# Kernel optimization log

Hardware: AMD Instinct MI355X
Metric: run time of the kernel (lower is better)

The kernel has to match this reference:

```python
import jax, jax.numpy as jnp
import numpy as np
import math

B, N, D, KA, H = 8, 1024, 512, 16, 8
QD = D // 4
HD = D // H


def qsplit(x):
    q = x.shape[-1] // 4
    return x[..., :q], x[..., q:2*q], x[..., 2*q:3*q], x[..., 3*q:]


def hprod(p, q):
    pr, pi, pj, pk = qsplit(p)
    qr, qi, qj, qk = qsplit(q)
    return jnp.concatenate([
        pr*qr - pi*qi - pj*qj - pk*qk,
        pr*qi + pi*qr + pj*qk - pk*qj,
        pr*qj - pi*qk + pj*qr + pk*qi,
        pr*qk + pi*qj - pj*qi + pk*qr,
    ], axis=-1)


def qconj(x):
    r, i, j, k = qsplit(x)
    return jnp.concatenate([r, -i, -j, -k], axis=-1)


def qlin(x, w, b):
    # w: [4, qo, qi] -> Hamilton block matrix [4qo, 4qi]
    r, i, j, k = w[0], w[1], w[2], w[3]
    W = jnp.concatenate([
        jnp.concatenate([r, -i, -j, -k], axis=1),
        jnp.concatenate([i,  r, -k,  j], axis=1),
        jnp.concatenate([j,  k,  r, -i], axis=1),
        jnp.concatenate([k, -j,  i,  r], axis=1),
    ], axis=0)
    return x @ W.T + b


def qln(x, gamma, beta):
    # per-component LayerNorm over Q; gamma/beta: [4, Q]
    qd = x.shape[-1] // 4
    xs = x.reshape(x.shape[:-1] + (4, qd))
    m = xs.mean(-1, keepdims=True)
    v = xs.var(-1, keepdims=True)
    y = (xs - m) / jnp.sqrt(v + 1e-5) * gamma + beta
    return y.reshape(x.shape)


def setup_inputs():
    key = jax.random.key(0)
    ks = jax.random.split(key, 20)
    lim = math.sqrt(6.0 / (2 * QD))  # xavier for [QD, QD]
    def qw(k):
        return jax.random.uniform(k, (4, QD, QD), minval=-lim, maxval=lim)
    return {
        'q': jax.random.normal(ks[0], (B, N, D), dtype=jnp.float32),
        'spike': jax.random.uniform(ks[1], (B, N), dtype=jnp.float32),
        'mask': jnp.ones((B, N), dtype=jnp.float32),
        'theta_logit': jnp.float32(0.0),
        'w_prim': qw(ks[2]), 'b_prim': jnp.zeros((D,), jnp.float32),
        'anchors': jax.random.normal(ks[3], (KA, D)) * 0.5,
        'log_sigma': jnp.zeros((KA,), jnp.float32),
        'w_aggr': qw(ks[4]), 'b_aggr': jnp.zeros((D,), jnp.float32),
        'w_q': qw(ks[5]), 'b_q': jnp.zeros((D,), jnp.float32),
        'w_k': qw(ks[6]), 'b_k': jnp.zeros((D,), jnp.float32),
        'w_v': qw(ks[7]), 'b_v': jnp.zeros((D,), jnp.float32),
        'w_o': qw(ks[8]), 'b_o': jnp.zeros((D,), jnp.float32),
        'ln_gamma': jnp.ones((4, QD), jnp.float32),
        'ln_beta': jnp.zeros((4, QD), jnp.float32),
    }


def reference(q, spike, mask, theta_logit, w_prim, b_prim, anchors, log_sigma,
              w_aggr, b_aggr, w_q, b_q, w_k, b_k, w_v, b_v, w_o, b_o,
              ln_gamma, ln_beta):
    b, n, d = q.shape
    qd = d // 4
    # --- SpikeQuaternionRotation: rotate toward K-axis by theta = theta_max*spike ---
    theta_max = (jnp.pi / 2) * jax.nn.sigmoid(theta_logit)
    theta = theta_max * spike                      # [B, N]
    c = jnp.cos(theta)[..., None]
    s = jnp.sin(theta)[..., None]
    z = jnp.zeros_like(c)
    rot = jnp.concatenate([
        jnp.broadcast_to(c, (b, n, qd)),
        jnp.broadcast_to(z, (b, n, qd)),
        jnp.broadcast_to(z, (b, n, qd)),
        jnp.broadcast_to(s, (b, n, qd)),
    ], axis=-1)
    q_rot = hprod(rot, q)                          # [B, N, D]

    # --- PrimaryLayer: per-cell quaternion transform ---
    msg_p = qlin(q_rot, w_prim, b_prim)

    # --- QuaternionAnchorLayer ---
    a_conj = qconj(anchors)                        # [KA, D]
    prod = hprod(q_rot[:, None, :, :], a_conj[None, :, None, :])  # [B, KA, N, D]
    dist = jnp.sum(prod * prod, axis=-1)           # [B, KA, N]
    sigma_sq = jnp.maximum(jnp.exp(log_sigma) ** 2, 1e-6)
    incid = jnp.exp(-dist / sigma_sq[None, :, None]) * mask[:, None, :]
    denom = jnp.maximum(incid.sum(-1, keepdims=True), 1e-6)
    h = jnp.einsum('bkn,bnd->bkd', incid, q_rot) / denom  # [B, KA, D]
    h = qlin(h, w_aggr, b_aggr)

    # --- QuaternionMHA(query=q_rot, key=h, value=h), no mask ---
    Qh = qlin(q_rot, w_q, b_q).reshape(b, n, H, HD)
    Kh = qlin(h, w_k, b_k).reshape(b, KA, H, HD)
    Vh = qlin(h, w_v, b_v).reshape(b, KA, H, HD)
    scores = jnp.einsum('bqhd,bkhd->bhqk', Qh, Kh) / jnp.sqrt(jnp.float32(HD))
    attn = jax.nn.softmax(scores, axis=-1)
    out = jnp.einsum('bhqk,bkhd->bqhd', attn, Vh).reshape(b, n, d)
    msg_a = qlin(out, w_o, b_o)

    # --- residual + per-component LayerNorm ---
    return qln(q + msg_p + msg_a, ln_gamma, ln_beta)
```

## Files before the change

### kernel.cpp

```cpp
#include <hip/hip_runtime.h>
#include <hip/hip_bf16.h>

typedef __hip_bfloat16 bf16;
typedef __attribute__((ext_vector_type(8))) short bf16x8;
typedef __attribute__((ext_vector_type(4))) float f32x4;

__device__ __forceinline__ float bflo(unsigned u) { return __uint_as_float(u << 16); }
__device__ __forceinline__ float bfhi(unsigned u) { return __uint_as_float(u & 0xffff0000u); }
__device__ __forceinline__ bool probe_f32(const void* mask) {
  return *(const unsigned*)mask == 0x3F800000u;
}
__device__ __forceinline__ float ldin(const void* p, size_t i, bool f32) {
  return f32 ? ((const float*)p)[i] : (float)((const bf16*)p)[i];
}

__global__ __launch_bounds__(256) void prologue(
    const void* w0, const void* w1, const void* w2, const void* w3,
    const void* w4, const void* w5,
    const void* b0, const void* b1, const void* b2, const void* b3,
    const void* b4, const void* b5, const void* g, const void* be,
    const void* q, const void* spike, const void* theta_logit, const void* mask,
    bf16* __restrict__ Wall, float* __restrict__ biasF,
    bf16* __restrict__ q_rot, float* __restrict__ qn) {
  bool f32 = probe_f32(mask);
  int blk = blockIdx.x, t = threadIdx.x;
  if (blk < 1536) {
    const int compT[4][4] = {{0,1,2,3},{1,0,3,2},{2,3,0,1},{3,2,1,0}};
    const float signT[4][4] = {{1.f,-1.f,-1.f,-1.f},{1.f,1.f,-1.f,1.f},{1.f,1.f,1.f,-1.f},{1.f,-1.f,1.f,1.f}};
    int E = blk * 1024 + t * 4;
    int wi = E >> 18;
    const void* src = wi == 0 ? w0 : wi == 1 ? w1 : wi == 2 ? w2 : wi == 3 ? w3 : wi == 4 ? w4 : w5;
    bf16 ov[4];
    #pragma unroll
    for (int j = 0; j < 4; ++j) {
      int e = (E + j) & 262143;
      int o = e >> 9, kk = e & 511;
      int ro = o >> 7, a = o & 127, co = kk >> 7, b2 = kk & 127;
      ov[j] = (bf16)(ldin(src, compT[ro][co] * 16384 + a * 128 + b2, f32) * signT[ro][co]);
    }
    *(uint2*)(Wall + E) = *(const uint2*)ov;
  } else if (blk < 1544) {
    int b = blk - 1536;
    const void* src = b == 0 ? b0 : b == 1 ? b1 : b == 2 ? b2 : b == 3 ? b3
                    : b == 4 ? b4 : b == 5 ? b5 : b == 6 ? g : be;
    biasF[b * 512 + t] = ldin(src, t, f32);
    biasF[b * 512 + 256 + t] = ldin(src, 256 + t, f32);
  } else {
    int row = (blk - 1544) * 2 + (t >> 7);
    int l = t & 127;
    float tl = ldin(theta_logit, 0, f32);
    float tmax = 1.5707963267948966f / (1.0f + __expf(-tl));
    float th = tmax * ldin(spike, row, f32);
    float c = cosf(th), s = sinf(th);
    size_t base = (size_t)row * 512;
    float a = ldin(q, base + l, f32), b = ldin(q, base + 128 + l, f32);
    float cc = ldin(q, base + 256 + l, f32), d = ldin(q, base + 384 + l, f32);
    float r0 = c * a - s * d;
    float r1 = c * b - s * cc;
    float r2 = c * cc + s * b;
    float r3 = c * d + s * a;
    bf16* orow = q_rot + base;
    orow[l] = (bf16)r0; orow[128 + l] = (bf16)r1; orow[256 + l] = (bf16)r2; orow[384 + l] = (bf16)r3;
    qn[(size_t)row * 128 + l] = r0 * r0 + r1 * r1 + r2 * r2 + r3 * r3;
  }
}

__device__ __forceinline__ void stage_B64(const bf16* __restrict__ Bw, int n0, char* Bs, int t) {
  int r = t & 63, cb = (t >> 6) * 16;
  const bf16* src = Bw + (size_t)(n0 + r) * 512;
  #pragma unroll
  for (int i = 0; i < 16; ++i) {
    int c = cb + i;
    int off = (c >> 2) * 4096 + (r >> 4) * 1024 + (((c & 3) * 16 + (r & 15)) * 16);
    *(uint4*)(Bs + off) = *(const uint4*)(src + c * 8);
  }
}

__global__ __launch_bounds__(256, 2) void gemm_dist(
    const bf16* __restrict__ A, const bf16* __restrict__ Bw,
    const float* __restrict__ bias0, const float* __restrict__ bias1,
    bf16* __restrict__ MQ,
    const float* __restrict__ qn, const void* anchors, const void* lsig,
    const void* mask, float* __restrict__ h_part, float* __restrict__ pd_part) {
  __shared__ char smem[77952];
  const int t = threadIdx.x;
  if (blockIdx.x >= 128) {
    char* Bs = smem;
    const int g = blockIdx.x - 128;
    const int wave = t >> 6, lane = t & 63;
    const int quad = lane >> 4, l16 = lane & 15;
    const int m0 = (g & 31) * 256, n0 = (g >> 5) * 64;
    stage_B64(Bw, n0, Bs, t);
    __syncthreads();
    const int mbase = m0 + wave * 64;
    f32x4 acc[4][4] = {};
    bf16x8 areg[2][4], breg[2][4];
    #pragma unroll
    for (int mt = 0; mt < 4; ++mt)
      areg[0][mt] = *(const bf16x8*)(A + (size_t)(mbase + mt * 16 + l16) * 512 + quad * 8);
    #pragma unroll
    for (int nt = 0; nt < 4; ++nt)
      breg[0][nt] = *(const bf16x8*)(Bs + nt * 1024 + lane * 16);
    #pragma unroll
    for (int kk = 0; kk < 16; ++kk) {
      const int cur = kk & 1, nxt = cur ^ 1;
      if (kk < 15) {
        const int k2 = (kk + 1) * 32;
        #pragma unroll
        for (int mt = 0; mt < 4; ++mt)
          areg[nxt][mt] = *(const bf16x8*)(A + (size_t)(mbase + mt * 16 + l16) * 512 + k2 + quad * 8);
        #pragma unroll
        for (int nt = 0; nt < 4; ++nt)
          breg[nxt][nt] = *(const bf16x8*)(Bs + (kk + 1) * 4096 + nt * 1024 + lane * 16);
      }
      #pragma unroll
      for (int mt = 0; mt < 4; ++mt)
        #pragma unroll
        for (int nt = 0; nt < 4; ++nt)
          acc[mt][nt] = __builtin_amdgcn_mfma_f32_16x16x32_bf16(areg[cur][mt], breg[cur][nt],
                                                                acc[mt][nt], 0, 0, 0);
    }
    #pragma unroll
    for (int nt = 0; nt < 4; ++nt) {
      int col = n0 + nt * 16 + l16;
      float bv = col < 512 ? bias0[col] : bias1[col - 512];
      #pragma unroll
      for (int mt = 0; mt < 4; ++mt) {
        int rb = mbase + mt * 16 + quad * 4;
        #pragma unroll
        for (int r = 0; r < 4; ++r)
          MQ[(size_t)(rb + r) * 1024 + col] = (bf16)(acc[mt][nt][r] + bv);
      }
    }
  } else {
    bool f32 = probe_f32(mask);
    bf16*  qr   = (bf16*)smem;
    float* an   = (float*)(smem + 65536);
    float* sInc = (float*)(smem + 73728);
    float* rs   = (float*)(smem + 77824);
    float* pd   = (float*)(smem + 77888);
    int bb = blockIdx.x;
    int b = bb >> 4, nc = bb & 15;
    {
      const uint4* src = (const uint4*)((const bf16*)A + ((size_t)b * 1024 + nc * 64) * 512);
      uint4* dst = (uint4*)qr;
      #pragma unroll
      for (int i = 0; i < 16; ++i) dst[t + i * 256] = src[t + i * 256];
    }
    for (int i = t; i < 2048; i += 256) {
      int k = i >> 7, l = i & 127;
      float a0 = ldin(anchors, k * 512 + l, f32);
      float a1 = ldin(anchors, k * 512 + 128 + l, f32);
      float a2 = ldin(anchors, k * 512 + 256 + l, f32);
      float a3 = ldin(anchors, k * 512 + 384 + l, f32);
      an[i] = a0 * a0 + a1 * a1 + a2 * a2 + a3 * a3;
    }
    if (t < 16) {
      float ls = ldin(lsig, t, f32);
      float ssq = __expf(ls); ssq = fmaxf(ssq * ssq, 1e-6f);
      rs[t] = -1.0f / ssq;
      pd[t] = 0.0f;
    }
    __syncthreads();
    {
      int rl = t >> 2, part = t & 3;
      int n = nc * 64 + rl;
      const float* qrow = qn + ((size_t)b * 1024 + n) * 128 + part * 32;
      f32x4 q4[8];
      #pragma unroll
      for (int i = 0; i < 8; ++i) q4[i] = *(const f32x4*)(qrow + i * 4);
      float sc[16] = {};
      #pragma unroll
      for (int i = 0; i < 8; ++i) {
        #pragma unroll
        for (int k = 0; k < 16; ++k) {
          f32x4 av = *(const f32x4*)(an + k * 128 + part * 32 + i * 4);
          sc[k] += q4[i][0] * av[0] + q4[i][1] * av[1] + q4[i][2] * av[2] + q4[i][3] * av[3];
        }
      }
      #pragma unroll
      for (int k = 0; k < 16; ++k) {
        sc[k] += __shfl_xor(sc[k], 1, 64);
        sc[k] += __shfl_xor(sc[k], 2, 64);
      }
      if (part == 0) {
        float mval = ldin(mask, b * 1024 + n, f32);
        #pragma unroll
        for (int k = 0; k < 16; ++k) {
          float inc = __expf(sc[k] * rs[k]) * mval;
          sInc[k * 64 + rl] = inc;
          atomicAdd(&pd[k], inc);
        }
      }
    }
    __syncthreads();
    {
      float acc0[16] = {}, acc1[16] = {};
      for (int nn = 0; nn < 64; ++nn) {
        float v0 = (float)qr[nn * 512 + t];
        float v1 = (float)qr[nn * 512 + 256 + t];
        #pragma unroll
        for (int k = 0; k < 16; ++k) {
          float p = sInc[k * 64 + nn];
          acc0[k] += p * v0;
          acc1[k] += p * v1;
        }
      }
      #pragma unroll
      for (int k = 0; k < 16; ++k) {
        size_t base = ((size_t)(b * 16 + k) * 16 + nc) * 512;
        h_part[base + t] = acc0[k];
        h_part[base + 256 + t] = acc1[k];
      }
    }
    if (t < 16) pd_part[((size_t)(b * 16 + t)) * 16 + nc] = pd[t];
  }
}

__global__ __launch_bounds__(256, 2) void gemm2(
    const bf16* __restrict__ A, const bf16* __restrict__ Bw,
    const float* __restrict__ biasO, bf16* __restrict__ msg_a) {
  __shared__ char Bs[65536];
  const int t = threadIdx.x;
  const int wave = t >> 6, lane = t & 63;
  const int quad = lane >> 4, l16 = lane & 15;
  const int m0 = blockIdx.x * 128, n0 = blockIdx.y * 64;
  stage_B64(Bw, n0, Bs, t);
  __syncthreads();
  const int mbase = m0 + wave * 32;
  f32x4 acc[2][4] = {};
  bf16x8 areg[2][2], breg[2][4];
  #pragma unroll
  for (int mt = 0; mt < 2; ++mt)
    areg[0][mt] = *(const bf16x8*)(A + (size_t)(mbase + mt * 16 + l16) * 512 + quad * 8);
  #pragma unroll
  for (int nt = 0; nt < 4; ++nt)
    breg[0][nt] = *(const bf16x8*)(Bs + nt * 1024 + lane * 16);
  #pragma unroll
  for (int kk = 0; kk < 16; ++kk) {
    const int cur = kk & 1, nxt = cur ^ 1;
    if (kk < 15) {
      const int k2 = (kk + 1) * 32;
      #pragma unroll
      for (int mt = 0; mt < 2; ++mt)
        areg[nxt][mt] = *(const bf16x8*)(A + (size_t)(mbase + mt * 16 + l16) * 512 + k2 + quad * 8);
      #pragma unroll
      for (int nt = 0; nt < 4; ++nt)
        breg[nxt][nt] = *(const bf16x8*)(Bs + (kk + 1) * 4096 + nt * 1024 + lane * 16);
    }
    #pragma unroll
    for (int mt = 0; mt < 2; ++mt)
      #pragma unroll
      for (int nt = 0; nt < 4; ++nt)
        acc[mt][nt] = __builtin_amdgcn_mfma_f32_16x16x32_bf16(areg[cur][mt], breg[cur][nt],
                                                              acc[mt][nt], 0, 0, 0);
  }
  #pragma unroll
  for (int nt = 0; nt < 4; ++nt) {
    int col = n0 + nt * 16 + l16;
    float bv = biasO[col];
    #pragma unroll
    for (int mt = 0; mt < 2; ++mt) {
      int rb = mbase + mt * 16 + quad * 4;
      #pragma unroll
      for (int r = 0; r < 4; ++r)
        msg_a[(size_t)(rb + r) * 512 + col] = (bf16)(acc[mt][nt][r] + bv);
    }
  }
}

__global__ __launch_bounds__(256) void qlin_akv(
    const float* __restrict__ h_part, const float* __restrict__ pd_part,
    const bf16* __restrict__ Wa, const float* __restrict__ ba,
    const bf16* __restrict__ Wk, const float* __restrict__ bk,
    const bf16* __restrict__ Wv, const float* __restrict__ bv,
    float* __restrict__ Kh, float* __restrict__ Vh) {
  __shared__ float xs[512];
  __shared__ float ys[512];
  int row = blockIdx.x, half = blockIdx.y;
  int t = threadIdx.x;
  float dsum = 0.0f;
  #pragma unroll
  for (int nc = 0; nc < 16; ++nc) dsum += pd_part[row * 16 + nc];
  float dinv = 1.0f / fmaxf(dsum, 1e-6f);
  #pragma unroll
  for (int j = 0; j < 2; ++j) {
    int d = j * 256 + t;
    float hv = 0.0f;
    #pragma unroll
    for (int nc = 0; nc < 16; ++nc) hv += h_part[(size_t)row * 8192 + nc * 512 + d];
    xs[d] = hv * dinv;
  }
  __syncthreads();
  #pragma unroll
  for (int j = 0; j < 2; ++j) {
    int o = j * 256 + t;
    const uint4* wr = (const uint4*)(Wa + (size_t)o * 512);
    float acc = ba[o];
    #pragma unroll 4
    for (int c = 0; c < 64; ++c) {
      uint4 u = wr[c];
      const float* xp = xs + c * 8;
      acc += xp[0] * bflo(u.x) + xp[1] * bfhi(u.x)
           + xp[2] * bflo(u.y) + xp[3] * bfhi(u.y)
           + xp[4] * bflo(u.z) + xp[5] * bfhi(u.z)
           + xp[6] * bflo(u.w) + xp[7] * bfhi(u.w);
    }
    ys[o] = acc;
  }
  __syncthreads();
  {
    int o = half * 256 + t;
    const uint4* wk = (const uint4*)(Wk + (size_t)o * 512);
    const uint4* wv = (const uint4*)(Wv + (size_t)o * 512);
    float ak = bk[o], av = bv[o];
    #pragma unroll 2
    for (int c = 0; c < 64; ++c) {
      uint4 uk = wk[c], uv = wv[c];
      const float* xp = ys + c * 8;
      ak += xp[0] * bflo(uk.x) + xp[1] * bfhi(uk.x)
          + xp[2] * bflo(uk.y) + xp[3] * bfhi(uk.y)
          + xp[4] * bflo(uk.z) + xp[5] * bfhi(uk.z)
          + xp[6] * bflo(uk.w) + xp[7] * bfhi(uk.w);
      av += xp[0] * bflo(uv.x) + xp[1] * bfhi(uv.x)
          + xp[2] * bflo(uv.y) + xp[3] * bfhi(uv.y)
          + xp[4] * bflo(uv.z) + xp[5] * bfhi(uv.z)
          + xp[6] * bflo(uv.w) + xp[7] * bfhi(uv.w);
    }
    Kh[(size_t)row * 512 + o] = ak;
    Vh[(size_t)row * 512 + o] = av;
  }
}

__global__ __launch_bounds__(256) void attn_v3(
    const bf16* __restrict__ MQ, const float* __restrict__ Kh_g,
    const float* __restrict__ Vh_g, bf16* __restrict__ attn_o) {
  __shared__ float KV[8 * 1092];
  __shared__ float P[16 * 132];
  const int t = threadIdx.x;
  const int rowbase = blockIdx.x * 16;
  const int b = rowbase >> 10;
  for (int i = t; i < 8192; i += 256) {
    int k = i >> 9, d = i & 511, h = d >> 6, dd = d & 63;
    KV[h * 1092 + k * 68 + dd] = Kh_g[(size_t)b * 8192 + i];
  }
  __syncthreads();
  {
    const int r = t >> 4, h = (t >> 1) & 7, hf = t & 1;
    const int grow = rowbase + r;
    const uint4* qp = (const uint4*)(MQ + (size_t)grow * 1024 + 512 + h * 64 + hf * 32);
    float q[32];
    #pragma unroll
    for (int i = 0; i < 4; ++i) {
      uint4 u = qp[i];
      q[i * 8 + 0] = bflo(u.x); q[i * 8 + 1] = bfhi(u.x);
      q[i * 8 + 2] = bflo(u.y); q[i * 8 + 3] = bfhi(u.y);
      q[i * 8 + 4] = bflo(u.z); q[i * 8 + 5] = bfhi(u.z);
      q[i * 8 + 6] = bflo(u.w); q[i * 8 + 7] = bfhi(u.w);
    }
    float sc[16];
    #pragma unroll
    for (int k = 0; k < 16; ++k) {
      float s = 0.0f;
      #pragma unroll
      for (int d4 = 0; d4 < 8; ++d4) {
        f32x4 kv = *(const f32x4*)(KV + h * 1092 + k * 68 + hf * 32 + d4 * 4);
        s += q[d4 * 4 + 0] * kv[0] + q[d4 * 4 + 1] * kv[1]
           + q[d4 * 4 + 2] * kv[2] + q[d4 * 4 + 3] * kv[3];
      }
      sc[k] = s;
    }
    #pragma unroll
    for (int k = 0; k < 16; ++k) sc[k] += __shfl_xor(sc[k], 1, 64);
    if (hf == 0) {
      #pragma unroll
      for (int k = 0; k < 16; ++k) sc[k] *= 0.125f;
      float m = sc[0];
      #pragma unroll
      for (int k = 1; k < 16; ++k) m = fmaxf(m, sc[k]);
      float ssum = 0.0f;
      #pragma unroll
      for (int k = 0; k < 16; ++k) { sc[k] = __expf(sc[k] - m); ssum += sc[k]; }
      float inv = 1.0f / ssum;
      #pragma unroll
      for (int k = 0; k < 16; ++k) P[r * 132 + h * 16 + k] = sc[k] * inv;
    }
  }
  __syncthreads();
  for (int i = t; i < 8192; i += 256) {
    int k = i >> 9, d = i & 511, h = d >> 6, dd = d & 63;
    KV[h * 1092 + k * 68 + dd] = Vh_g[(size_t)b * 8192 + i];
  }
  __syncthreads();
  {
    const int r = t >> 4, dg = t & 15;
    #pragma unroll
    for (int h = 0; h < 8; ++h) {
      float a0 = 0, a1 = 0, a2 = 0, a3 = 0;
      #pragma unroll
      for (int k = 0; k < 16; ++k) {
        float p = P[r * 132 + h * 16 + k];
        f32x4 va = *(const f32x4*)(KV + h * 1092 + k * 68 + dg * 4);
        a0 += p * va[0]; a1 += p * va[1]; a2 += p * va[2]; a3 += p * va[3];
      }
      bf16 ov[4] = {(bf16)a0, (bf16)a1, (bf16)a2, (bf16)a3};
      *(uint2*)(attn_o + (size_t)(rowbase + r) * 512 + h * 64 + dg * 4) = *(const uint2*)ov;
    }
  }
}

__global__ __launch_bounds__(256) void ln_v2(
    const void* q, const void* mask, const bf16* __restrict__ MQ,
    const bf16* __restrict__ msg_a, const float* __restrict__ gamF, void* out) {
  bool f32 = probe_f32(mask);
  int t = threadIdx.x;
  int row = blockIdx.x * 2 + (t >> 7);
  int l = t & 127;
  int e0 = l * 4;
  float x[4];
  {
    uint2 um = *(const uint2*)(MQ + (size_t)row * 1024 + e0);
    uint2 ua = *(const uint2*)(msg_a + (size_t)row * 512 + e0);
    float qv[4];
    if (f32) {
      f32x4 qq = *(const f32x4*)((const float*)q + (size_t)row * 512 + e0);
      qv[0] = qq[0]; qv[1] = qq[1]; qv[2] = qq[2]; qv[3] = qq[3];
    } else {
      uint2 uq = *(const uint2*)((const bf16*)q + (size_t)row * 512 + e0);
      qv[0] = bflo(uq.x); qv[1] = bfhi(uq.x); qv[2] = bflo(uq.y); qv[3] = bfhi(uq.y);
    }
    x[0] = qv[0] + bflo(um.x) + bflo(ua.x);
    x[1] = qv[1] + bfhi(um.x) + bfhi(ua.x);
    x[2] = qv[2] + bflo(um.y) + bflo(ua.y);
    x[3] = qv[3] + bfhi(um.y) + bfhi(ua.y);
  }
  float s = x[0] + x[1] + x[2] + x[3];
  float s2 = x[0] * x[0] + x[1] * x[1] + x[2] * x[2] + x[3] * x[3];
  #pragma unroll
  for (int off = 1; off <= 16; off <<= 1) {
    s  += __shfl_xor(s, off, 64);
    s2 += __shfl_xor(s2, off, 64);
  }
  float m = s * (1.0f / 128.0f);
  float rinv = rsqrtf(s2 * (1.0f / 128.0f) - m * m + 1e-5f);
  f32x4 ga = *(const f32x4*)(gamF + e0);
  f32x4 be = *(const f32x4*)(gamF + 512 + e0);
  float y[4];
  #pragma unroll
  for (int j = 0; j < 4; ++j) y[j] = (x[j] - m) * rinv * ga[j] + be[j];
  if (f32) {
    f32x4 ov = {y[0], y[1], y[2], y[3]};
    *(f32x4*)((float*)out + (size_t)row * 512 + e0) = ov;
  } else {
    bf16 ov[4] = {(bf16)y[0], (bf16)y[1], (bf16)y[2], (bf16)y[3]};
    *(uint2*)((bf16*)out + (size_t)row * 512 + e0) = *(const uint2*)ov;
  }
}

extern "C" void kernel_launch(void* const* d_in, const int* in_sizes, int n_in,
                              void* d_out, int out_size, void* d_ws, size_t ws_size,
                              hipStream_t stream) {
  (void)in_sizes; (void)n_in; (void)out_size; (void)ws_size;
  const void* q      = d_in[0];
  const void* spike  = d_in[1];
  const void* mask   = d_in[2];
  const void* tl     = d_in[3];
  const void* w_prim = d_in[4];
  const void* b_prim = d_in[5];
  const void* anchors= d_in[6];
  const void* lsig   = d_in[7];
  const void* w_aggr = d_in[8];
  const void* b_aggr = d_in[9];
  const void* w_q    = d_in[10];
  const void* b_q    = d_in[11];
  const void* w_k    = d_in[12];
  const void* b_k    = d_in[13];
  const void* w_v    = d_in[14];
  const void* b_v    = d_in[15];
  const void* w_o    = d_in[16];
  const void* b_o    = d_in[17];
  const void* gam    = d_in[18];
  const void* bet    = d_in[19];

  char* ws = (char*)d_ws;
  bf16*  Wall   = (bf16*)(ws + 0);
  bf16*  q_rot  = (bf16*)(ws + 3145728);
  float* qn     = (float*)(ws + 11534336);
  bf16*  MQ     = (bf16*)(ws + 15728640);
  float* h_part = (float*)(ws + 32505856);
  float* pd_part= (float*)(ws + 36700160);
  float* Kh     = (float*)(ws + 36708352);
  float* Vh     = (float*)(ws + 36970496);
  bf16*  attn_o = (bf16*)(ws + 37232640);
  bf16*  msg_a  = (bf16*)(ws + 45621248);
  float* biasF  = (float*)(ws + 54009856);

  prologue<<<5640, 256, 0, stream>>>(w_prim, w_q, w_o, w_aggr, w_k, w_v,
                                     b_prim, b_q, b_o, b_aggr, b_k, b_v, gam, bet,
                                     q, spike, tl, mask, Wall, biasF, q_rot, qn);
  gemm_dist<<<640, 256, 0, stream>>>(q_rot, Wall, biasF + 0, biasF + 512, MQ,
                                     qn, anchors, lsig, mask, h_part, pd_part);
  qlin_akv<<<dim3(128, 2), 256, 0, stream>>>(h_part, pd_part,
                                             Wall + 3 * 262144, biasF + 1536,
                                             Wall + 4 * 262144, biasF + 2048,
                                             Wall + 5 * 262144, biasF + 2560, Kh, Vh);
  attn_v3<<<512, 256, 0, stream>>>(MQ, Kh, Vh, attn_o);
  gemm2<<<dim3(64, 8), 256, 0, stream>>>(attn_o, Wall + 2 * 262144, biasF + 1024, msg_a);
  ln_v2<<<4096, 256, 0, stream>>>(q, mask, MQ, msg_a, biasF + 3072, d_out);
}
```

Before: 213.6 us.

## Fuse all stages into one persistent cooperative kernel with grid syncs

Replaces the six separate kernel launches with a single persistent cooperative kernel. Each stage runs as a grid-stride loop over jobs, separated by grid.sync(). If the cooperative launch fails, the code falls back to the original multi-kernel path. This removes launch overhead and inter-kernel gaps, but the fixed grid of up to 512 blocks may load-balance worse than the original grids, and grid-wide barriers have their own cost.

```diff
diff --git a/kernel.cpp b/kernel.cpp
--- a/kernel.cpp
+++ b/kernel.cpp
@@ -1,5 +1,8 @@
 #include <hip/hip_runtime.h>
 #include <hip/hip_bf16.h>
+#include <hip/hip_cooperative_groups.h>
+
+namespace cg = cooperative_groups;
 
 typedef __hip_bfloat16 bf16;
 typedef __attribute__((ext_vector_type(8))) short bf16x8;
@@ -14,22 +17,25 @@
   return f32 ? ((const float*)p)[i] : (float)((const bf16*)p)[i];
 }
 
-__global__ __launch_bounds__(256) void prologue(
-    const void* w0, const void* w1, const void* w2, const void* w3,
-    const void* w4, const void* w5,
-    const void* b0, const void* b1, const void* b2, const void* b3,
-    const void* b4, const void* b5, const void* g, const void* be,
-    const void* q, const void* spike, const void* theta_logit, const void* mask,
-    bf16* __restrict__ Wall, float* __restrict__ biasF,
-    bf16* __restrict__ q_rot, float* __restrict__ qn) {
-  bool f32 = probe_f32(mask);
-  int blk = blockIdx.x, t = threadIdx.x;
+struct MegaArgs {
+  const void *q, *spike, *mask, *tl;
+  const void *w0, *w1, *w2, *w3, *w4, *w5;
+  const void *b0, *b1, *b2, *b3, *b4, *b5, *g, *be;
+  const void *anchors, *lsig;
+  bf16* Wall; float* biasF; bf16* q_rot; float* qn;
+  bf16* MQ; float* h_part; float* pd_part; float* Kh; float* Vh;
+  bf16* attn_o; bf16* msg_a; void* out;
+};
+
+
+__device__ __forceinline__ void prologue_job(const MegaArgs& A, bool f32, int blk, int t) {
   if (blk < 1536) {
     const int compT[4][4] = {{0,1,2,3},{1,0,3,2},{2,3,0,1},{3,2,1,0}};
     const float signT[4][4] = {{1.f,-1.f,-1.f,-1.f},{1.f,1.f,-1.f,1.f},{1.f,1.f,1.f,-1.f},{1.f,-1.f,1.f,1.f}};
     int E = blk * 1024 + t * 4;
     int wi = E >> 18;
-    const void* src = wi == 0 ? w0 : wi == 1 ? w1 : wi == 2 ? w2 : wi == 3 ? w3 : wi == 4 ? w4 : w5;
+    const void* src = wi == 0 ? A.w0 : wi == 1 ? A.w1 : wi == 2 ? A.w2
+                    : wi == 3 ? A.w3 : wi == 4 ? A.w4 : A.w5;
     bf16 ov[4];
     #pragma unroll
     for (int j = 0; j < 4; ++j) {
@@ -38,30 +44,30 @@
       int ro = o >> 7, a = o & 127, co = kk >> 7, b2 = kk & 127;
       ov[j] = (bf16)(ldin(src, compT[ro][co] * 16384 + a * 128 + b2, f32) * signT[ro][co]);
     }
-    *(uint2*)(Wall + E) = *(const uint2*)ov;
+    *(uint2*)(A.Wall + E) = *(const uint2*)ov;
   } else if (blk < 1544) {
     int b = blk - 1536;
-    const void* src = b == 0 ? b0 : b == 1 ? b1 : b == 2 ? b2 : b == 3 ? b3
-                    : b == 4 ? b4 : b == 5 ? b5 : b == 6 ? g : be;
-    biasF[b * 512 + t] = ldin(src, t, f32);
-    biasF[b * 512 + 256 + t] = ldin(src, 256 + t, f32);
+    const void* src = b == 0 ? A.b0 : b == 1 ? A.b1 : b == 2 ? A.b2 : b == 3 ? A.b3
+                    : b == 4 ? A.b4 : b == 5 ? A.b5 : b == 6 ? A.g : A.be;
+    A.biasF[b * 512 + t] = ldin(src, t, f32);
+    A.biasF[b * 512 + 256 + t] = ldin(src, 256 + t, f32);
   } else {
     int row = (blk - 1544) * 2 + (t >> 7);
     int l = t & 127;
-    float tl = ldin(theta_logit, 0, f32);
+    float tl = ldin(A.tl, 0, f32);
     float tmax = 1.5707963267948966f / (1.0f + __expf(-tl));
-    float th = tmax * ldin(spike, row, f32);
+    float th = tmax * ldin(A.spike, row, f32);
     float c = cosf(th), s = sinf(th);
     size_t base = (size_t)row * 512;
-    float a = ldin(q, base + l, f32), b = ldin(q, base + 128 + l, f32);
-    float cc = ldin(q, base + 256 + l, f32), d = ldin(q, base + 384 + l, f32);
+    float a = ldin(A.q, base + l, f32), b = ldin(A.q, base + 128 + l, f32);
+    float cc = ldin(A.q, base + 256 + l, f32), d = ldin(A.q, base + 384 + l, f32);
     float r0 = c * a - s * d;
     float r1 = c * b - s * cc;
     float r2 = c * cc + s * b;
     float r3 = c * d + s * a;
-    bf16* orow = q_rot + base;
+    bf16* orow = A.q_rot + base;
     orow[l] = (bf16)r0; orow[128 + l] = (bf16)r1; orow[256 + l] = (bf16)r2; orow[384 + l] = (bf16)r3;
-    qn[(size_t)row * 128 + l] = r0 * r0 + r1 * r1 + r2 * r2 + r3 * r3;
+    A.qn[(size_t)row * 128 + l] = r0 * r0 + r1 * r1 + r2 * r2 + r3 * r3;
   }
 }
 
@@ -76,163 +82,23 @@
   }
 }
 
-__global__ __launch_bounds__(256, 2) void gemm_dist(
-    const bf16* __restrict__ A, const bf16* __restrict__ Bw,
+__device__ __forceinline__ void gemm1_tile(
+    const bf16* __restrict__ Aq, const bf16* __restrict__ Bw,
     const float* __restrict__ bias0, const float* __restrict__ bias1,
-    bf16* __restrict__ MQ,
-    const float* __restrict__ qn, const void* anchors, const void* lsig,
-    const void* mask, float* __restrict__ h_part, float* __restrict__ pd_part) {
-  __shared__ char smem[77952];
-  const int t = threadIdx.x;
-  if (blockIdx.x >= 128) {
-    char* Bs = smem;
-    const int g = blockIdx.x - 128;
-    const int wave = t >> 6, lane = t & 63;
-    const int quad = lane >> 4, l16 = lane & 15;
-    const int m0 = (g & 31) * 256, n0 = (g >> 5) * 64;
-    stage_B64(Bw, n0, Bs, t);
-    __syncthreads();
-    const int mbase = m0 + wave * 64;
-    f32x4 acc[4][4] = {};
-    bf16x8 areg[2][4], breg[2][4];
-    #pragma unroll
-    for (int mt = 0; mt < 4; ++mt)
-      areg[0][mt] = *(const bf16x8*)(A + (size_t)(mbase + mt * 16 + l16) * 512 + quad * 8);
-    #pragma unroll
-    for (int nt = 0; nt < 4; ++nt)
-      breg[0][nt] = *(const bf16x8*)(Bs + nt * 1024 + lane * 16);
-    #pragma unroll
-    for (int kk = 0; kk < 16; ++kk) {
-      const int cur = kk & 1, nxt = cur ^ 1;
-      if (kk < 15) {
-        const int k2 = (kk + 1) * 32;
-        #pragma unroll
-        for (int mt = 0; mt < 4; ++mt)
-          areg[nxt][mt] = *(const bf16x8*)(A + (size_t)(mbase + mt * 16 + l16) * 512 + k2 + quad * 8);
-        #pragma unroll
-        for (int nt = 0; nt < 4; ++nt)
-          breg[nxt][nt] = *(const bf16x8*)(Bs + (kk + 1) * 4096 + nt * 1024 + lane * 16);
-      }
-      #pragma unroll
-      for (int mt = 0; mt < 4; ++mt)
-        #pragma unroll
-        for (int nt = 0; nt < 4; ++nt)
-          acc[mt][nt] = __builtin_amdgcn_mfma_f32_16x16x32_bf16(areg[cur][mt], breg[cur][nt],
-                                                                acc[mt][nt], 0, 0, 0);
-    }
-    #pragma unroll
-    for (int nt = 0; nt < 4; ++nt) {
-      int col = n0 + nt * 16 + l16;
-      float bv = col < 512 ? bias0[col] : bias1[col - 512];
-      #pragma unroll
-      for (int mt = 0; mt < 4; ++mt) {
-        int rb = mbase + mt * 16 + quad * 4;
-        #pragma unroll
-        for (int r = 0; r < 4; ++r)
-          MQ[(size_t)(rb + r) * 1024 + col] = (bf16)(acc[mt][nt][r] + bv);
-      }
-    }
-  } else {
-    bool f32 = probe_f32(mask);
-    bf16*  qr   = (bf16*)smem;
-    float* an   = (float*)(smem + 65536);
-    float* sInc = (float*)(smem + 73728);
-    float* rs   = (float*)(smem + 77824);
-    float* pd   = (float*)(smem + 77888);
-    int bb = blockIdx.x;
-    int b = bb >> 4, nc = bb & 15;
-    {
-      const uint4* src = (const uint4*)((const bf16*)A + ((size_t)b * 1024 + nc * 64) * 512);
-      uint4* dst = (uint4*)qr;
-      #pragma unroll
-      for (int i = 0; i < 16; ++i) dst[t + i * 256] = src[t + i * 256];
-    }
-    for (int i = t; i < 2048; i += 256) {
-      int k = i >> 7, l = i & 127;
-      float a0 = ldin(anchors, k * 512 + l, f32);
-      float a1 = ldin(anchors, k * 512 + 128 + l, f32);
-      float a2 = ldin(anchors, k * 512 + 256 + l, f32);
-      float a3 = ldin(anchors, k * 512 + 384 + l, f32);
-      an[i] = a0 * a0 + a1 * a1 + a2 * a2 + a3 * a3;
-    }
-    if (t < 16) {
-      float ls = ldin(lsig, t, f32);
-      float ssq = __expf(ls); ssq = fmaxf(ssq * ssq, 1e-6f);
-      rs[t] = -1.0f / ssq;
-      pd[t] = 0.0f;
-    }
-    __syncthreads();
-    {
-      int rl = t >> 2, part = t & 3;
-      int n = nc * 64 + rl;
-      const float* qrow = qn + ((size_t)b * 1024 + n) * 128 + part * 32;
-      f32x4 q4[8];
-      #pragma unroll
-      for (int i = 0; i < 8; ++i) q4[i] = *(const f32x4*)(qrow + i * 4);
-      float sc[16] = {};
-      #pragma unroll
-      for (int i = 0; i < 8; ++i) {
-        #pragma unroll
-        for (int k = 0; k < 16; ++k) {
-          f32x4 av = *(const f32x4*)(an + k * 128 + part * 32 + i * 4);
-          sc[k] += q4[i][0] * av[0] + q4[i][1] * av[1] + q4[i][2] * av[2] + q4[i][3] * av[3];
-        }
-      }
-      #pragma unroll
-      for (int k = 0; k < 16; ++k) {
-        sc[k] += __shfl_xor(sc[k], 1, 64);
-        sc[k] += __shfl_xor(sc[k], 2, 64);
-      }
-      if (part == 0) {
-        float mval = ldin(mask, b * 1024 + n, f32);
-        #pragma unroll
-        for (int k = 0; k < 16; ++k) {
-          float inc = __expf(sc[k] * rs[k]) * mval;
-          sInc[k * 64 + rl] = inc;
-          atomicAdd(&pd[k], inc);
-        }
-      }
-    }
-    __syncthreads();
-    {
-      float acc0[16] = {}, acc1[16] = {};
-      for (int nn = 0; nn < 64; ++nn) {
-        float v0 = (float)qr[nn * 512 + t];
-        float v1 = (float)qr[nn * 512 + 256 + t];
-        #pragma unroll
-        for (int k = 0; k < 16; ++k) {
-          float p = sInc[k * 64 + nn];
-          acc0[k] += p * v0;
-          acc1[k] += p * v1;
-        }
-      }
-      #pragma unroll
-      for (int k = 0; k < 16; ++k) {
-        size_t base = ((size_t)(b * 16 + k) * 16 + nc) * 512;
-        h_part[base + t] = acc0[k];
-        h_part[base + 256 + t] = acc1[k];
-      }
-    }
-    if (t < 16) pd_part[((size_t)(b * 16 + t)) * 16 + nc] = pd[t];
-  }
-}
-
-__global__ __launch_bounds__(256, 2) void gemm2(
-    const bf16* __restrict__ A, const bf16* __restrict__ Bw,
-    const float* __restrict__ biasO, bf16* __restrict__ msg_a) {
-  __shared__ char Bs[65536];
-  const int t = threadIdx.x;
+    bf16* __restrict__ MQ, char* smem, int g, int t) {
+  char* Bs = smem;
   const int wave = t >> 6, lane = t & 63;
   const int quad = lane >> 4, l16 = lane & 15;
-  const int m0 = blockIdx.x * 128, n0 = blockIdx.y * 64;
+  const int m0 = (g & 31) * 256, n0 = (g >> 5) * 64;
+  __syncthreads();
   stage_B64(Bw, n0, Bs, t);
   __syncthreads();
-  const int mbase = m0 + wave * 32;
-  f32x4 acc[2][4] = {};
-  bf16x8 areg[2][2], breg[2][4];
-  #pragma unroll
-  for (int mt = 0; mt < 2; ++mt)
-    areg[0][mt] = *(const bf16x8*)(A + (size_t)(mbase + mt * 16 + l16) * 512 + quad * 8);
+  const int mbase = m0 + wave * 64;
+  f32x4 acc[4][4] = {};
+  bf16x8 areg[2][4], breg[2][4];
+  #pragma unroll
+  for (int mt = 0; mt < 4; ++mt)
+    areg[0][mt] = *(const bf16x8*)(Aq + (size_t)(mbase + mt * 16 + l16) * 512 + quad * 8);
   #pragma unroll
   for (int nt = 0; nt < 4; ++nt)
     breg[0][nt] = *(const bf16x8*)(Bs + nt * 1024 + lane * 16);
@@ -242,14 +108,14 @@
     if (kk < 15) {
       const int k2 = (kk + 1) * 32;
       #pragma unroll
-      for (int mt = 0; mt < 2; ++mt)
-        areg[nxt][mt] = *(const bf16x8*)(A + (size_t)(mbase + mt * 16 + l16) * 512 + k2 + quad * 8);
+      for (int mt = 0; mt < 4; ++mt)
+        areg[nxt][mt] = *(const bf16x8*)(Aq + (size_t)(mbase + mt * 16 + l16) * 512 + k2 + quad * 8);
       #pragma unroll
       for (int nt = 0; nt < 4; ++nt)
         breg[nxt][nt] = *(const bf16x8*)(Bs + (kk + 1) * 4096 + nt * 1024 + lane * 16);
     }
     #pragma unroll
-    for (int mt = 0; mt < 2; ++mt)
+    for (int mt = 0; mt < 4; ++mt)
       #pragma unroll
       for (int nt = 0; nt < 4; ++nt)
         acc[mt][nt] = __builtin_amdgcn_mfma_f32_16x16x32_bf16(areg[cur][mt], breg[cur][nt],
@@ -258,37 +124,121 @@
   #pragma unroll
   for (int nt = 0; nt < 4; ++nt) {
     int col = n0 + nt * 16 + l16;
-    float bv = biasO[col];
-    #pragma unroll
-    for (int mt = 0; mt < 2; ++mt) {
+    float bv = col < 512 ? bias0[col] : bias1[col - 512];
+    #pragma unroll
+    for (int mt = 0; mt < 4; ++mt) {
       int rb = mbase + mt * 16 + quad * 4;
       #pragma unroll
       for (int r = 0; r < 4; ++r)
-        msg_a[(size_t)(rb + r) * 512 + col] = (bf16)(acc[mt][nt][r] + bv);
-    }
-  }
-}
-
-__global__ __launch_bounds__(256) void qlin_akv(
-    const float* __restrict__ h_part, const float* __restrict__ pd_part,
-    const bf16* __restrict__ Wa, const float* __restrict__ ba,
-    const bf16* __restrict__ Wk, const float* __restrict__ bk,
-    const bf16* __restrict__ Wv, const float* __restrict__ bv,
-    float* __restrict__ Kh, float* __restrict__ Vh) {
-  __shared__ float xs[512];
-  __shared__ float ys[512];
-  int row = blockIdx.x, half = blockIdx.y;
-  int t = threadIdx.x;
+        MQ[(size_t)(rb + r) * 1024 + col] = (bf16)(acc[mt][nt][r] + bv);
+    }
+  }
+}
+
+__device__ __forceinline__ void dist_job(const MegaArgs& Ar, bool f32, char* smem, int bb, int t) {
+  bf16*  qr   = (bf16*)smem;
+  float* an   = (float*)(smem + 65536);
+  float* sInc = (float*)(smem + 73728);
+  float* rs   = (float*)(smem + 77824);
+  float* pd   = (float*)(smem + 77888);
+  int b = bb >> 4, nc = bb & 15;
+  __syncthreads();
+  {
+    const uint4* src = (const uint4*)((const bf16*)Ar.q_rot + ((size_t)b * 1024 + nc * 64) * 512);
+    uint4* dst = (uint4*)qr;
+    #pragma unroll
+    for (int i = 0; i < 16; ++i) dst[t + i * 256] = src[t + i * 256];
+  }
+  for (int i = t; i < 2048; i += 256) {
+    int k = i >> 7, l = i & 127;
+    float a0 = ldin(Ar.anchors, k * 512 + l, f32);
+    float a1 = ldin(Ar.anchors, k * 512 + 128 + l, f32);
+    float a2 = ldin(Ar.anchors, k * 512 + 256 + l, f32);
+    float a3 = ldin(Ar.anchors, k * 512 + 384 + l, f32);
+    an[i] = a0 * a0 + a1 * a1 + a2 * a2 + a3 * a3;
+  }
+  if (t < 16) {
+    float ls = ldin(Ar.lsig, t, f32);
+    float ssq = __expf(ls); ssq = fmaxf(ssq * ssq, 1e-6f);
+    rs[t] = -1.0f / ssq;
+    pd[t] = 0.0f;
+  }
+  __syncthreads();
+  {
+    int rl = t >> 2, part = t & 3;
+    int n = nc * 64 + rl;
+    const float* qrow = Ar.qn + ((size_t)b * 1024 + n) * 128 + part * 32;
+    f32x4 q4[8];
+    #pragma unroll
+    for (int i = 0; i < 8; ++i) q4[i] = *(const f32x4*)(qrow + i * 4);
+    float sc[16] = {};
+    #pragma unroll
+    for (int i = 0; i < 8; ++i) {
+      #pragma unroll
+      for (int k = 0; k < 16; ++k) {
+        f32x4 av = *(const f32x4*)(an + k * 128 + part * 32 + i * 4);
+        sc[k] += q4[i][0] * av[0] + q4[i][1] * av[1] + q4[i][2] * av[2] + q4[i][3] * av[3];
+      }
+    }
+    #pragma unroll
+    for (int k = 0; k < 16; ++k) {
+      sc[k] += __shfl_xor(sc[k], 1, 64);
+      sc[k] += __shfl_xor(sc[k], 2, 64);
+    }
+    if (part == 0) {
+      float mval = ldin(Ar.mask, b * 1024 + n, f32);
+      #pragma unroll
+      for (int k = 0; k < 16; ++k) {
+        float inc = __expf(sc[k] * rs[k]) * mval;
+        sInc[k * 64 + rl] = inc;
+        atomicAdd(&pd[k], inc);
+      }
+    }
+  }
+  __syncthreads();
+  {
+    float acc0[16] = {}, acc1[16] = {};
+    for (int nn = 0; nn < 64; ++nn) {
+      float v0 = (float)qr[nn * 512 + t];
+      float v1 = (float)qr[nn * 512 + 256 + t];
+      #pragma unroll
+      for (int k = 0; k < 16; ++k) {
+        float p = sInc[k * 64 + nn];
+        acc0[k] += p * v0;
+        acc1[k] += p * v1;
+      }
+    }
+    #pragma unroll
+    for (int k = 0; k < 16; ++k) {
+      size_t base = ((size_t)(b * 16 + k) * 16 + nc) * 512;
+      Ar.h_part[base + t] = acc0[k];
+      Ar.h_part[base + 256 + t] = acc1[k];
+    }
+  }
+  if (t < 16) Ar.pd_part[((size_t)(b * 16 + t)) * 16 + nc] = pd[t];
+}
+
+__device__ __forceinline__ void qlin_job(const MegaArgs& A, char* smem, int job, int t) {
+  float* xs = (float*)smem;
+  float* ys = (float*)(smem + 2048);
+  const bf16* Wa = A.Wall + 3 * 262144;
+  const bf16* Wk = A.Wall + 4 * 262144;
+  const bf16* Wv = A.Wall + 5 * 262144;
+  const float* ba = A.biasF + 1536;
+  const float* bk = A.biasF + 2048;
+  const float* bv = A.biasF + 2560;
+  int row = job >> 1, half = job & 1;
+  __syncthreads();
   float dsum = 0.0f;
   #pragma unroll
-  for (int nc = 0; nc < 16; ++nc) dsum += pd_part[row * 16 + nc];
+  for (int nc = 0; nc < 16; ++nc) dsum += A.pd_part[row * 16 + nc];
   float dinv = 1.0f / fmaxf(dsum, 1e-6f);
   #pragma unroll
   for (int j = 0; j < 2; ++j) {
     int d = j * 256 + t;
     float hv = 0.0f;
     #pragma unroll
-    for (int nc = 0; nc < 16; ++nc) hv += h_part[(size_t)row * 8192 + nc * 512 + d];
+    for (int nc = 0; nc < 16; ++nc) hv += A.h_part[(size_t)row * 8192 + nc * 512 + d];
     xs[d] = hv * dinv;
   }
   __syncthreads();
@@ -327,28 +277,26 @@
           + xp[4] * bflo(uv.z) + xp[5] * bfhi(uv.z)
           + xp[6] * bflo(uv.w) + xp[7] * bfhi(uv.w);
     }
-    Kh[(size_t)row * 512 + o] = ak;
-    Vh[(size_t)row * 512 + o] = av;
-  }
-}
-
-__global__ __launch_bounds__(256) void attn_v3(
-    const bf16* __restrict__ MQ, const float* __restrict__ Kh_g,
-    const float* __restrict__ Vh_g, bf16* __restrict__ attn_o) {
-  __shared__ float KV[8 * 1092];
-  __shared__ float P[16 * 132];
-  const int t = threadIdx.x;
-  const int rowbase = blockIdx.x * 16;
+    A.Kh[(size_t)row * 512 + o] = ak;
+    A.Vh[(size_t)row * 512 + o] = av;
+  }
+}
+
+__device__ __forceinline__ void attn_job(const MegaArgs& A, char* smem, int job, int t) {
+  float* KV = (float*)smem;
+  float* P  = (float*)(smem + 34944);
+  const int rowbase = job * 16;
   const int b = rowbase >> 10;
+  __syncthreads();
   for (int i = t; i < 8192; i += 256) {
     int k = i >> 9, d = i & 511, h = d >> 6, dd = d & 63;
-    KV[h * 1092 + k * 68 + dd] = Kh_g[(size_t)b * 8192 + i];
+    KV[h * 1092 + k * 68 + dd] = A.Kh[(size_t)b * 8192 + i];
   }
   __syncthreads();
   {
     const int r = t >> 4, h = (t >> 1) & 7, hf = t & 1;
     const int grow = rowbase + r;
-    const uint4* qp = (const uint4*)(MQ + (size_t)grow * 1024 + 512 + h * 64 + hf * 32);
+    const uint4* qp = (const uint4*)(A.MQ + (size_t)grow * 1024 + 512 + h * 64 + hf * 32);
     float q[32];
     #pragma unroll
     for (int i = 0; i < 4; ++i) {
@@ -389,7 +337,7 @@
   __syncthreads();
   for (int i = t; i < 8192; i += 256) {
     int k = i >> 9, d = i & 511, h = d >> 6, dd = d & 63;
-    KV[h * 1092 + k * 68 + dd] = Vh_g[(size_t)b * 8192 + i];
+    KV[h * 1092 + k * 68 + dd] = A.Vh[(size_t)b * 8192 + i];
   }
   __syncthreads();
   {
@@ -404,29 +352,78 @@
         a0 += p * va[0]; a1 += p * va[1]; a2 += p * va[2]; a3 += p * va[3];
       }
       bf16 ov[4] = {(bf16)a0, (bf16)a1, (bf16)a2, (bf16)a3};
-      *(uint2*)(attn_o + (size_t)(rowbase + r) * 512 + h * 64 + dg * 4) = *(const uint2*)ov;
-    }
-  }
-}
-
-__global__ __launch_bounds__(256) void ln_v2(
-    const void* q, const void* mask, const bf16* __restrict__ MQ,
-    const bf16* __restrict__ msg_a, const float* __restrict__ gamF, void* out) {
-  bool f32 = probe_f32(mask);
-  int t = threadIdx.x;
-  int row = blockIdx.x * 2 + (t >> 7);
+      *(uint2*)(A.attn_o + (size_t)(rowbase + r) * 512 + h * 64 + dg * 4) = *(const uint2*)ov;
+    }
+  }
+}
+
+__device__ __forceinline__ void gemm2_tile(
+    const bf16* __restrict__ Ai, const bf16* __restrict__ Bw,
+    const float* __restrict__ biasO, bf16* __restrict__ msg_a, char* smem, int job, int t) {
+  char* Bs = smem;
+  const int wave = t >> 6, lane = t & 63;
+  const int quad = lane >> 4, l16 = lane & 15;
+  const int m0 = (job & 63) * 128, n0 = (job >> 6) * 64;
+  __syncthreads();
+  stage_B64(Bw, n0, Bs, t);
+  __syncthreads();
+  const int mbase = m0 + wave * 32;
+  f32x4 acc[2][4] = {};
+  bf16x8 areg[2][2], breg[2][4];
+  #pragma unroll
+  for (int mt = 0; mt < 2; ++mt)
+    areg[0][mt] = *(const bf16x8*)(Ai + (size_t)(mbase + mt * 16 + l16) * 512 + quad * 8);
+  #pragma unroll
+  for (int nt = 0; nt < 4; ++nt)
+    breg[0][nt] = *(const bf16x8*)(Bs + nt * 1024 + lane * 16);
+  #pragma unroll
+  for (int kk = 0; kk < 16; ++kk) {
+    const int cur = kk & 1, nxt = cur ^ 1;
+    if (kk < 15) {
+      const int k2 = (kk + 1) * 32;
+      #pragma unroll
+      for (int mt = 0; mt < 2; ++mt)
+        areg[nxt][mt] = *(const bf16x8*)(Ai + (size_t)(mbase + mt * 16 + l16) * 512 + k2 + quad * 8);
+      #pragma unroll
+      for (int nt = 0; nt < 4; ++nt)
+        breg[nxt][nt] = *(const bf16x8*)(Bs + (kk + 1) * 4096 + nt * 1024 + lane * 16);
+    }
+    #pragma unroll
+    for (int mt = 0; mt < 2; ++mt)
+      #pragma unroll
+      for (int nt = 0; nt < 4; ++nt)
+        acc[mt][nt] = __builtin_amdgcn_mfma_f32_16x16x32_bf16(areg[cur][mt], breg[cur][nt],
+                                                              acc[mt][nt], 0, 0, 0);
+  }
+  #pragma unroll
+  for (int nt = 0; nt < 4; ++nt) {
+    int col = n0 + nt * 16 + l16;
+    float bv = biasO[col];
+    #pragma unroll
+    for (int mt = 0; mt < 2; ++mt) {
+      int rb = mbase + mt * 16 + quad * 4;
+      #pragma unroll
+      for (int r = 0; r < 4; ++r)
+        msg_a[(size_t)(rb + r) * 512 + col] = (bf16)(acc[mt][nt][r] + bv);
+    }
+  }
+}
+
+__device__ __forceinline__ void ln_job(const MegaArgs& A, bool f32, int job, int t) {
+  int row = job * 2 + (t >> 7);
   int l = t & 127;
   int e0 = l * 4;
+  const float* gamF = A.biasF + 3072;
   float x[4];
   {
-    uint2 um = *(const uint2*)(MQ + (size_t)row * 1024 + e0);
-    uint2 ua = *(const uint2*)(msg_a + (size_t)row * 512 + e0);
+    uint2 um = *(const uint2*)(A.MQ + (size_t)row * 1024 + e0);
+    uint2 ua = *(const uint2*)(A.msg_a + (size_t)row * 512 + e0);
     float qv[4];
     if (f32) {
-      f32x4 qq = *(const f32x4*)((const float*)q + (size_t)row * 512 + e0);
+      f32x4 qq = *(const f32x4*)((const float*)A.q + (size_t)row * 512 + e0);
       qv[0] = qq[0]; qv[1] = qq[1]; qv[2] = qq[2]; qv[3] = qq[3];
     } else {
-      uint2 uq = *(const uint2*)((const bf16*)q + (size_t)row * 512 + e0);
+      uint2 uq = *(const uint2*)((const bf16*)A.q + (size_t)row * 512 + e0);
       qv[0] = bflo(uq.x); qv[1] = bfhi(uq.x); qv[2] = bflo(uq.y); qv[3] = bfhi(uq.y);
     }
     x[0] = qv[0] + bflo(um.x) + bflo(ua.x);
@@ -450,61 +447,115 @@
   for (int j = 0; j < 4; ++j) y[j] = (x[j] - m) * rinv * ga[j] + be[j];
   if (f32) {
     f32x4 ov = {y[0], y[1], y[2], y[3]};
-    *(f32x4*)((float*)out + (size_t)row * 512 + e0) = ov;
+    *(f32x4*)((float*)A.out + (size_t)row * 512 + e0) = ov;
   } else {
     bf16 ov[4] = {(bf16)y[0], (bf16)y[1], (bf16)y[2], (bf16)y[3]};
-    *(uint2*)((bf16*)out + (size_t)row * 512 + e0) = *(const uint2*)ov;
-  }
+    *(uint2*)((bf16*)A.out + (size_t)row * 512 + e0) = *(const uint2*)ov;
+  }
+}
+
+__global__ __launch_bounds__(256, 2) void mega(MegaArgs A) {
+  __shared__ char smem[77952];
+  cg::grid_group grid = cg::this_grid();
+  const int nb = (int)gridDim.x;
+  const int gid = (int)blockIdx.x;
+  const int t = (int)threadIdx.x;
+  const bool f32 = probe_f32(A.mask);
+
+  for (int blk = gid; blk < 5640; blk += nb) prologue_job(A, f32, blk, t);
+  grid.sync();
+
+  for (int g = gid; g < 512; g += nb)
+    gemm1_tile(A.q_rot, A.Wall, A.biasF, A.biasF + 512, A.MQ, smem, g, t);
+  for (int bb = gid; bb < 128; bb += nb) dist_job(A, f32, smem, bb, t);
+  grid.sync();
+
+  for (int job = gid; job < 256; job += nb) qlin_job(A, smem, job, t);
+  grid.sync();
+
+  for (int job = gid; job < 512; job += nb) attn_job(A, smem, job, t);
+  grid.sync();
+
+  for (int job = gid; job < 512; job += nb)
+    gemm2_tile(A.attn_o, A.Wall + 2 * 262144, A.biasF + 1024, A.msg_a, smem, job, t);
+  grid.sync();
+
+  for (int job = gid; job < 4096; job += nb) ln_job(A, f32, job, t);
+}
+
+__global__ __launch_bounds__(256) void k_prologue(MegaArgs A) {
+  bool f32 = probe_f32(A.mask);
+  prologue_job(A, f32, blockIdx.x, threadIdx.x);
+}
+__global__ __launch_bounds__(256, 2) void k_gemm_dist(MegaArgs A) {
+  __shared__ char smem[77952];
+  bool f32 = probe_f32(A.mask);
+  if (blockIdx.x >= 128)
+    gemm1_tile(A.q_rot, A.Wall, A.biasF, A.biasF + 512, A.MQ, smem, blockIdx.x - 128, threadIdx.x);
+  else
+    dist_job(A, f32, smem, blockIdx.x, threadIdx.x);
+}
+__global__ __launch_bounds__(256) void k_qlin(MegaArgs A) {
+  __shared__ char smem[4096];
+  qlin_job(A, smem, blockIdx.x, threadIdx.x);
+}
+__global__ __launch_bounds__(256) void k_attn(MegaArgs A) {
+  __shared__ char smem[43392];
+  attn_job(A, smem, blockIdx.x, threadIdx.x);
+}
+__global__ __launch_bounds__(256, 2) void k_gemm2(MegaArgs A) {
+  __shared__ char smem[65536];
+  gemm2_tile(A.attn_o, A.Wall + 2 * 262144, A.biasF + 1024, A.msg_a, smem, blockIdx.x, threadIdx.x);
+}
+__global__ __launch_bounds__(256) void k_ln(MegaArgs A) {
+  bool f32 = probe_f32(A.mask);
+  ln_job(A, f32, blockIdx.x, threadIdx.x);
 }
 
 extern "C" void kernel_launch(void* const* d_in, const int* in_sizes, int n_in,
                               void* d_out, int out_size, void* d_ws, size_t ws_size,
                               hipStream_t stream) {
   (void)in_sizes; (void)n_in; (void)out_size; (void)ws_size;
-  const void* q      = d_in[0];
-  const void* spike  = d_in[1];
-  const void* mask   = d_in[2];
-  const void* tl     = d_in[3];
-  const void* w_prim = d_in[4];
-  const void* b_prim = d_in[5];
-  const void* anchors= d_in[6];
-  const void* lsig   = d_in[7];
-  const void* w_aggr = d_in[8];
-  const void* b_aggr = d_in[9];
-  const void* w_q    = d_in[10];
-  const void* b_q    = d_in[11];
-  const void* w_k    = d_in[12];
-  const void* b_k    = d_in[13];
-  const void* w_v    = d_in[14];
-  const void* b_v    = d_in[15];
-  const void* w_o    = d_in[16];
-  const void* b_o    = d_in[17];
-  const void* gam    = d_in[18];
-  const void* bet    = d_in[19];
-
   char* ws = (char*)d_ws;
-  bf16*  Wall   = (bf16*)(ws + 0);
-  bf16*  q_rot  = (bf16*)(ws + 3145728);
-  float* qn     = (float*)(ws + 11534336);
-  bf16*  MQ     = (bf16*)(ws + 15728640);
-  float* h_part = (float*)(ws + 32505856);
-  float* pd_part= (float*)(ws + 36700160);
-  float* Kh     = (float*)(ws + 36708352);
-  float* Vh     = (float*)(ws + 36970496);
-  bf16*  attn_o = (bf16*)(ws + 37232640);
-  bf16*  msg_a  = (bf16*)(ws + 45621248);
-  float* biasF  = (float*)(ws + 54009856);
-
-  prologue<<<5640, 256, 0, stream>>>(w_prim, w_q, w_o, w_aggr, w_k, w_v,
-                                     b_prim, b_q, b_o, b_aggr, b_k, b_v, gam, bet,
-                                     q, spike, tl, mask, Wall, biasF, q_rot, qn);
-  gemm_dist<<<640, 256, 0, stream>>>(q_rot, Wall, biasF + 0, biasF + 512, MQ,
-                                     qn, anchors, lsig, mask, h_part, pd_part);
-  qlin_akv<<<dim3(128, 2), 256, 0, stream>>>(h_part, pd_part,
-                                             Wall + 3 * 262144, biasF + 1536,
-                                             Wall + 4 * 262144, biasF + 2048,
-                                             Wall + 5 * 262144, biasF + 2560, Kh, Vh);
-  attn_v3<<<512, 256, 0, stream>>>(MQ, Kh, Vh, attn_o);
-  gemm2<<<dim3(64, 8), 256, 0, stream>>>(attn_o, Wall + 2 * 262144, biasF + 1024, msg_a);
-  ln_v2<<<4096, 256, 0, stream>>>(q, mask, MQ, msg_a, biasF + 3072, d_out);
-}
+  MegaArgs h;
+  h.q = d_in[0];  h.spike = d_in[1]; h.mask = d_in[2]; h.tl = d_in[3];
+  h.w0 = d_in[4]; h.b0 = d_in[5];
+  h.anchors = d_in[6]; h.lsig = d_in[7];
+  h.w3 = d_in[8]; h.b3 = d_in[9];
+  h.w1 = d_in[10]; h.b1 = d_in[11];
+  h.w4 = d_in[12]; h.b4 = d_in[13];
+  h.w5 = d_in[14]; h.b5 = d_in[15];
+  h.w2 = d_in[16]; h.b2 = d_in[17];
+  h.g = d_in[18]; h.be = d_in[19];
+  h.Wall    = (bf16*)(ws + 0);
+  h.q_rot   = (bf16*)(ws + 3145728);
+  h.qn      = (float*)(ws + 11534336);
+  h.MQ      = (bf16*)(ws + 15728640);
+  h.h_part  = (float*)(ws + 32505856);
+  h.pd_part = (float*)(ws + 36700160);
+  h.Kh      = (float*)(ws + 36708352);
+  h.Vh      = (float*)(ws + 36970496);
+  h.attn_o  = (bf16*)(ws + 37232640);
+  h.msg_a   = (bf16*)(ws + 45621248);
+  h.biasF   = (float*)(ws + 54009856);
+  h.out     = d_out;
+
+  int maxB = 0;
+  if (hipOccupancyMaxActiveBlocksPerMultiprocessor(&maxB, (const void*)mega, 256, 0) != hipSuccess)
+    maxB = 0;
+  if (maxB < 1) maxB = 1;
+  int grid = maxB * 256;
+  if (grid > 512) grid = 512;
+
+  void* params[1] = { (void*)&h };
+  hipError_t err = hipLaunchCooperativeKernel((const void*)mega, dim3(grid), dim3(256),
+                                              params, 0, stream);
+  if (err != hipSuccess) {
+    k_prologue<<<5640, 256, 0, stream>>>(h);
+    k_gemm_dist<<<640, 256, 0, stream>>>(h);
+    k_qlin<<<256, 256, 0, stream>>>(h);
+    k_attn<<<512, 256, 0, stream>>>(h);
+    k_gemm2<<<512, 256, 0, stream>>>(h);
+    k_ln<<<4096, 256, 0, stream>>>(h);
+  }
+}
```

Result: slower. 426.8 us (+99.9%).
